# Kernel optimization log

Hardware: AMD Instinct MI355X
Metric: run time of the kernel (lower is better)

## Reference

```python
import jax, jax.numpy as jnp
import numpy as np

# Filter hyperparameters from init_kwargs (cv2.bilateralFilter semantics)
D = 9
RADIUS = D // 2
SIGMA_COLOR = 75.0
SIGMA_SPACE = 75.0


def setup_inputs() -> dict:
    key = jax.random.key(0)
    # batch of RGB images in [0, 255] like a typical cv2 float image
    sample = jax.random.uniform(key, (8, 1024, 1024, 3), dtype=jnp.float32) * 255.0
    return {"sample": sample}


def _bilateral(sample):
    B, H, W, C = sample.shape
    r = RADIUS
    color_coeff = -0.5 / (SIGMA_COLOR * SIGMA_COLOR)
    space_coeff = -0.5 / (SIGMA_SPACE * SIGMA_SPACE)
    # OpenCV default border: BORDER_REFLECT_101 == numpy 'reflect'
    padded = jnp.pad(sample, ((0, 0), (r, r), (r, r), (0, 0)), mode="reflect")

    num = jnp.zeros_like(sample)                      # [B,H,W,C]
    den = jnp.zeros(sample.shape[:3], sample.dtype)   # [B,H,W]
    # Fixed, small unrolled loop over window taps (not a data-dim loop).
    for dy in range(-r, r + 1):
        for dx in range(-r, r + 1):
            r2 = dy * dy + dx * dx
            if r2 > r * r:  # OpenCV restricts taps to the inscribed circle
                continue
            sw = np.exp(space_coeff * r2).astype(np.float32)
            nb = padded[:, r + dy : r + dy + H, r + dx : r + dx + W, :]  # [B,H,W,C]
            # OpenCV color distance: L1 norm over channels, squared in the Gaussian
            diff = jnp.sum(jnp.abs(nb - sample), axis=-1)  # [B,H,W]
            w = sw * jnp.exp(color_coeff * diff * diff)    # [B,H,W]
            num = num + w[..., None] * nb
            den = den + w
    return num / den[..., None]


def reference(sample):
    return _bilateral(sample)
```

## Files before the change

### kernel.cpp

```cpp
#include <hip/hip_runtime.h>


namespace {
constexpr int Himg = 1024;
constexpr int Wimg = 1024;
constexpr int CHN  = 3;
constexpr int RAD  = 4;

constexpr int BXT = 64;
constexpr int BYT = 4;
constexpr int TW  = BXT + 2 * RAD;
constexpr int TH  = BYT + 2 * RAD;
constexpr int NPX = TW * TH;

constexpr float LOG2E = 1.4426950408889634f;
constexpr float COEFF = -0.5f / (75.0f * 75.0f);
constexpr float KC2   = COEFF * LOG2E;

typedef float f4 __attribute__((ext_vector_type(4)));
}

__device__ __forceinline__ int reflect_idx(int i, int n) {
    i = (i < 0) ? -i : i;
    return (i >= n) ? (2 * n - 2 - i) : i;
}

__global__ __launch_bounds__(256, 4)
void bilateral_kernel(const float* __restrict__ in, float* __restrict__ out) {
    __shared__ f4 tile[TH][TW];

    const float SC     = sqrtf(-KC2);
    const float INV_SC = 1.0f / SC;

    const int tid = threadIdx.x;
    const int x0  = blockIdx.x * BXT;
    const int y0  = blockIdx.y * BYT;

    const float* __restrict__ img = in + (size_t)blockIdx.z * Himg * Wimg * CHN;

    for (int i = tid; i < NPX; i += 256) {
        const int row = i / TW;
        const int px  = i - row * TW;
        const int gy  = reflect_idx(y0 - RAD + row, Himg);
        const int gx  = reflect_idx(x0 - RAD + px,  Wimg);
        const float* p = img + ((size_t)gy * Wimg + gx) * CHN;
        f4 v;
        v.x = p[0] * SC;
        v.y = p[1] * SC;
        v.z = p[2] * SC;
        v.w = 1.0f;
        tile[row][px] = v;
    }
    __syncthreads();

    const int tx = tid & 63;
    const int ty = tid >> 6;

    const f4 c = tile[ty + RAD][tx + RAD];
    const float cx = c.x, cy = c.y, cz = c.z;

    f4 acc = (f4){0.0f, 0.0f, 0.0f, 0.0f};

#pragma unroll
    for (int dy = -RAD; dy <= RAD; ++dy) {
#pragma unroll
        for (int dx = -RAD; dx <= RAD; ++dx) {
            const int r2 = dy * dy + dx * dx;
            if (r2 > RAD * RAD) continue;

            const f4 nb = tile[ty + RAD + dy][tx + RAD + dx];

            const float diff = fabsf(nb.x - cx) + fabsf(nb.y - cy)
                             + fabsf(nb.z - cz);

            const float w = __builtin_amdgcn_exp2f(
                fmaf(diff, -diff, KC2 * (float)r2));

            acc += nb * w;
        }
    }

    const float inv = (1.0f / acc.w) * INV_SC;
    const size_t o =
        ((size_t)(blockIdx.z * Himg + y0 + ty) * Wimg + (x0 + tx)) * CHN;
    out[o + 0] = acc.x * inv;
    out[o + 1] = acc.y * inv;
    out[o + 2] = acc.z * inv;
}

extern "C" void kernel_launch(void* const* d_in, const int* in_sizes, int n_in,
                              void* d_out, int out_size, void* d_ws, size_t ws_size,
                              hipStream_t stream) {
    const float* in = (const float*)d_in[0];
    float* out = (float*)d_out;

    const int B = in_sizes[0] / (Himg * Wimg * CHN);

    dim3 grid(Wimg / BXT, Himg / BYT, B);
    dim3 block(256);
    bilateral_kernel<<<grid, block, 0, stream>>>(in, out);
}
```

Baseline: 254.0 us.

## Compute two vertically adjacent output pixels per thread sharing LDS neighbor loads

Each thread now produces two output rows, so the tile height doubles and each block covers eight rows. Every neighbor pixel read from shared memory serves both centers where the circular windows overlap. This cuts LDS reads per output and shrinks the halo fraction of the tile. The cost is more registers for the second accumulator and center, a larger shared tile that may lower occupancy, and half as many blocks.

```diff
diff --git a/kernel.cpp b/kernel.cpp
--- a/kernel.cpp
+++ b/kernel.cpp
@@ -8,7 +8,8 @@
 constexpr int RAD  = 4;
 
 constexpr int BXT = 64;
-constexpr int BYT = 4;
+constexpr int PV  = 2;
+constexpr int BYT = 4 * PV;
 constexpr int TW  = BXT + 2 * RAD;
 constexpr int TH  = BYT + 2 * RAD;
 constexpr int NPX = TW * TH;
@@ -18,11 +19,24 @@
 constexpr float KC2   = COEFF * LOG2E;
 
 typedef float f4 __attribute__((ext_vector_type(4)));
+
+constexpr int lim(int dy) {
+    int a = dy < 0 ? -dy : dy;
+    return a == 0 ? 4 : a == 1 ? 3 : a == 2 ? 3 : a == 3 ? 2 : a == 4 ? 0 : -1;
+}
+constexpr int cmax(int a, int b) { return a > b ? a : b; }
 }
 
 __device__ __forceinline__ int reflect_idx(int i, int n) {
     i = (i < 0) ? -i : i;
     return (i >= n) ? (2 * n - 2 - i) : i;
+}
+
+__device__ __forceinline__ void tap(f4& acc, const f4& c, const f4& nb,
+                                    float kr2) {
+    const float diff = fabsf(nb.x - c.x) + fabsf(nb.y - c.y) + fabsf(nb.z - c.z);
+    const float w = __builtin_amdgcn_exp2f(fmaf(diff, -diff, kr2));
+    acc += nb * w;
 }
 
 __global__ __launch_bounds__(256, 4)
@@ -53,39 +67,46 @@
     }
     __syncthreads();
 
-    const int tx = tid & 63;
-    const int ty = tid >> 6;
+    const int tx  = tid & 63;
+    const int wv  = tid >> 6;
+    const int ly0 = wv * PV;
 
-    const f4 c = tile[ty + RAD][tx + RAD];
-    const float cx = c.x, cy = c.y, cz = c.z;
+    const f4 cA = tile[ly0 + RAD + 0][tx + RAD];
+    const f4 cB = tile[ly0 + RAD + 1][tx + RAD];
 
-    f4 acc = (f4){0.0f, 0.0f, 0.0f, 0.0f};
+    f4 aA = (f4){0.f, 0.f, 0.f, 0.f};
+    f4 aB = (f4){0.f, 0.f, 0.f, 0.f};
 
 #pragma unroll
-    for (int dy = -RAD; dy <= RAD; ++dy) {
+    for (int sr = 0; sr < PV + 2 * RAD; ++sr) {
+        const int dyA = sr - RAD;
+        const int dyB = sr - RAD - 1;
+        const int LA  = lim(dyA);
+        const int LB  = lim(dyB);
+        const int L   = cmax(LA, LB);
 #pragma unroll
         for (int dx = -RAD; dx <= RAD; ++dx) {
-            const int r2 = dy * dy + dx * dx;
-            if (r2 > RAD * RAD) continue;
-
-            const f4 nb = tile[ty + RAD + dy][tx + RAD + dx];
-
-            const float diff = fabsf(nb.x - cx) + fabsf(nb.y - cy)
-                             + fabsf(nb.z - cz);
-
-            const float w = __builtin_amdgcn_exp2f(
-                fmaf(diff, -diff, KC2 * (float)r2));
-
-            acc += nb * w;
+            if (dx < -L || dx > L) continue;
+            const f4 nb = tile[ly0 + sr][tx + RAD + dx];
+            if (dx >= -LA && dx <= LA)
+                tap(aA, cA, nb, KC2 * (float)(dyA * dyA + dx * dx));
+            if (dx >= -LB && dx <= LB)
+                tap(aB, cB, nb, KC2 * (float)(dyB * dyB + dx * dx));
         }
     }
 
-    const float inv = (1.0f / acc.w) * INV_SC;
-    const size_t o =
-        ((size_t)(blockIdx.z * Himg + y0 + ty) * Wimg + (x0 + tx)) * CHN;
-    out[o + 0] = acc.x * inv;
-    out[o + 1] = acc.y * inv;
-    out[o + 2] = acc.z * inv;
+    const size_t oA =
+        ((size_t)(blockIdx.z * Himg + y0 + ly0) * Wimg + (x0 + tx)) * CHN;
+    const float invA = (1.0f / aA.w) * INV_SC;
+    out[oA + 0] = aA.x * invA;
+    out[oA + 1] = aA.y * invA;
+    out[oA + 2] = aA.z * invA;
+
+    const size_t oB = oA + (size_t)Wimg * CHN;
+    const float invB = (1.0f / aB.w) * INV_SC;
+    out[oB + 0] = aB.x * invB;
+    out[oB + 1] = aB.y * invB;
+    out[oB + 2] = aB.z * invB;
 }
 
 extern "C" void kernel_launch(void* const* d_in, const int* in_sizes, int n_in,
```

Result: slower. 500.5 us (+97.0%).
